# Performance work log

Measured on AMD Instinct MI355X. Metric: run time of the kernel, lower is better.

The kernel has to match this reference:

```python
import jax, jax.numpy as jnp
import numpy as np

EMBED_DIM = 1024
NUM_HEADS = 16
HEAD_DIM = EMBED_DIM // NUM_HEADS


def setup_inputs() -> dict:
    key = jax.random.key(0)
    k1, k2, k3, k4, k5 = jax.random.split(key, 5)
    B, S, D = 2, 2048, EMBED_DIM
    s_in = 1.0 / np.sqrt(D)
    x = jax.random.normal(k1, (B, S, D), dtype=jnp.float32)
    W_qkv = jax.random.uniform(k2, (D, 3 * D), dtype=jnp.float32, minval=-s_in, maxval=s_in)
    b_qkv = jax.random.uniform(k3, (3 * D,), dtype=jnp.float32, minval=-s_in, maxval=s_in)
    W_out = jax.random.uniform(k4, (D, D), dtype=jnp.float32, minval=-s_in, maxval=s_in)
    b_out = jax.random.uniform(k5, (D,), dtype=jnp.float32, minval=-s_in, maxval=s_in)
    return {"x": x, "W_qkv": W_qkv, "b_qkv": b_qkv, "W_out": W_out, "b_out": b_out}


def reference(x, W_qkv, b_qkv, W_out, b_out):
    B, S, D = x.shape
    H, Hd = NUM_HEADS, HEAD_DIM
    qkv = x @ W_qkv + b_qkv                      # [B,S,3D]
    qkv = qkv.reshape(B, S, 3, H, Hd)
    q = qkv[:, :, 0].transpose(0, 2, 1, 3)       # [B,H,S,Hd]
    k = qkv[:, :, 1].transpose(0, 2, 1, 3)
    v = qkv[:, :, 2].transpose(0, 2, 1, 3)
    scores = jnp.einsum('bhsd,bhtd->bhst', q, k) / jnp.sqrt(jnp.float32(Hd))
    attn = jax.nn.softmax(scores, axis=-1)       # dropout is identity in eval mode
    out = jnp.einsum('bhst,bhtd->bhsd', attn, v)
    out = out.transpose(0, 2, 1, 3).reshape(B, S, D)
    return out @ W_out + b_out
```

## Files before the change

### kernel.cpp

```cpp
#include <hip/hip_runtime.h>
#include <stdint.h>
#include <math.h>

#define EMBED 1024
#define HEADS 16
#define HDIM  64
#define SEQ   2048
#define BATCH 2

typedef __bf16 bf16x8 __attribute__((ext_vector_type(8)));
typedef float  f32x4  __attribute__((ext_vector_type(4)));
typedef unsigned short u16x8 __attribute__((ext_vector_type(8)));
typedef unsigned short u16x4 __attribute__((ext_vector_type(4)));
typedef uint32_t u32x4v __attribute__((ext_vector_type(4)));

static __device__ __forceinline__ unsigned short f2bf(float f){
  union { float f; uint32_t u; } v; v.f = f;
  uint32_t u = v.u;
  uint32_t r = (u + 0x7FFFu + ((u >> 16) & 1u)) >> 16;
  return (unsigned short)r;
}
static __device__ __forceinline__ bf16x8 as_bf(u16x8 v){ return __builtin_bit_cast(bf16x8, v); }

static __device__ __forceinline__ uint32_t pk_bf16(float a, float b){
#if defined(__has_builtin) && __has_builtin(__builtin_amdgcn_cvt_pk_bf16_f32)
  typedef __bf16 bf16x2 __attribute__((ext_vector_type(2)));
  bf16x2 p = __builtin_amdgcn_cvt_pk_bf16_f32(a, b);
  return __builtin_bit_cast(uint32_t, p);
#else
  return (uint32_t)f2bf(a) | ((uint32_t)f2bf(b) << 16);
#endif
}

static __device__ __forceinline__ float fexp2(float x){
#if defined(__has_builtin) && __has_builtin(__builtin_amdgcn_exp2f)
  return __builtin_amdgcn_exp2f(x);
#else
  return exp2f(x);
#endif
}

static __device__ __forceinline__ void stage16(const unsigned short* gp,
                                               unsigned short* lp_wave, int lane){
#if defined(__has_builtin) && __has_builtin(__builtin_amdgcn_global_load_lds)
  __builtin_amdgcn_global_load_lds((const __attribute__((address_space(1))) void*)gp,
                                   (__attribute__((address_space(3))) void*)lp_wave,
                                   16, 0, 0);
#else
  *(u16x8*)(lp_wave + lane * 8) = *(const u16x8*)gp;
#endif
}

__global__ __launch_bounds__(256) void cast_x(const float* __restrict__ in,
                                              unsigned short* __restrict__ out){
  int i = (blockIdx.x * 256 + threadIdx.x) * 4;
  float4 v = *(const float4*)(in + i);
  u16x4 o;
  o[0] = f2bf(v.x); o[1] = f2bf(v.y); o[2] = f2bf(v.z); o[3] = f2bf(v.w);
  *(u16x4*)(out + i) = o;
}

__global__ __launch_bounds__(256) void wtrans(const float* __restrict__ W,
                                              unsigned short* __restrict__ Wt,
                                              int N, int K){
  __shared__ unsigned short T[32 * 36];
  int t = threadIdx.x;
  int n0 = blockIdx.x * 32, k0 = blockIdx.y * 32;
  int kr = t >> 3, nc = (t & 7) * 4;
  float4 wv = *(const float4*)(W + (size_t)(k0 + kr) * N + n0 + nc);
  T[(nc + 0) * 36 + kr] = f2bf(wv.x);
  T[(nc + 1) * 36 + kr] = f2bf(wv.y);
  T[(nc + 2) * 36 + kr] = f2bf(wv.z);
  T[(nc + 3) * 36 + kr] = f2bf(wv.w);
  __syncthreads();
  int nr = t >> 3, kc = (t & 7) * 4;
  *(u16x4*)(Wt + (size_t)(n0 + nr) * K + k0 + kc) = *(const u16x4*)&T[nr * 36 + kc];
}

__global__ __launch_bounds__(256) void vtrans(const unsigned short* __restrict__ V,
                                              unsigned short* __restrict__ VT){
  __shared__ unsigned short T[32 * 36];
  int t = threadIdx.x;
  int s0 = blockIdx.x * 32, d0 = blockIdx.y * 32;
  size_t base = (size_t)blockIdx.z * SEQ * HDIM;
  int sr = t >> 3, dc = (t & 7) * 4;
  u16x4 vv = *(const u16x4*)(V + base + (size_t)(s0 + sr) * HDIM + d0 + dc);
  T[(dc + 0) * 36 + sr] = vv[0];
  T[(dc + 1) * 36 + sr] = vv[1];
  T[(dc + 2) * 36 + sr] = vv[2];
  T[(dc + 3) * 36 + sr] = vv[3];
  __syncthreads();
  int dr = t >> 3, sc = (t & 7) * 4;
  int pos = (((sc >> 2) & 3) << 3) + (((sc >> 4) & 1) << 2);
  *(u16x4*)(VT + base + (size_t)(d0 + dr) * SEQ + s0 + pos) = *(const u16x4*)&T[dr * 36 + sc];
}

template<int MODE>
__global__ __launch_bounds__(256) void gemm_bf16(
    const unsigned short* __restrict__ A,
    const unsigned short* __restrict__ Bt,
    const float* __restrict__ bias,
    float* __restrict__ Cout,
    unsigned short* __restrict__ q_ws,
    unsigned short* __restrict__ k_ws,
    unsigned short* __restrict__ v_ws,
    int M, int N, int K)
{
  __shared__ unsigned short As[128 * 32];
  __shared__ unsigned short Bs[128 * 32];
  const int tid  = threadIdx.x;
  const int bm   = blockIdx.y, bn = blockIdx.x;
  const int w    = tid >> 6, lane = tid & 63;
  const int quad = lane >> 4, l16 = lane & 15;
  const int wm   = (w >> 1) * 64, wn = (w & 1) * 64;

  f32x4 acc[4][4] = {};

  for (int k0 = 0; k0 < K; k0 += 32) {
    #pragma unroll
    for (int i = 0; i < 2; i++){
      int c = w + i * 4;
      int row = c * 16 + (lane >> 2);
      int kg = (lane & 3) ^ (row & 3);
      stage16(A  + (size_t)(bm * 128 + row) * K + k0 + kg * 8, &As[c * 512], lane);
      stage16(Bt + (size_t)(bn * 128 + row) * K + k0 + kg * 8, &Bs[c * 512], lane);
    }
    __syncthreads();

    bf16x8 af[4], bfr[4];
    #pragma unroll
    for (int t = 0; t < 4; t++){
      int ra = wm + t * 16 + l16;
      int rb = wn + t * 16 + l16;
      af[t]  = as_bf(*(const u16x8*)&As[(ra << 5) + ((quad ^ (ra & 3)) << 3)]);
      bfr[t] = as_bf(*(const u16x8*)&Bs[(rb << 5) + ((quad ^ (rb & 3)) << 3)]);
    }
    #pragma unroll
    for (int mt = 0; mt < 4; mt++)
      #pragma unroll
      for (int nt = 0; nt < 4; nt++)
        acc[mt][nt] = __builtin_amdgcn_mfma_f32_16x16x32_bf16(af[mt], bfr[nt], acc[mt][nt], 0, 0, 0);
    __syncthreads();
  }

  #pragma unroll
  for (int mt = 0; mt < 4; mt++){
    #pragma unroll
    for (int nt = 0; nt < 4; nt++){
      #pragma unroll
      for (int r = 0; r < 4; r++){
        int gm = bm * 128 + wm + mt * 16 + quad * 4 + r;
        int gn = bn * 128 + wn + nt * 16 + l16;
        float val = acc[mt][nt][r] + bias[gn];
        if (MODE == 0){
          int which = gn >> 10, rem = gn & 1023;
          int h = rem >> 6, hd = rem & 63;
          int b = gm >> 11, s = gm & 2047;
          size_t off = ((size_t)(b * HEADS + h) * SEQ + s) * HDIM + hd;
          if (which == 0)      q_ws[off] = f2bf(val * 0.18033688f);
          else if (which == 1) k_ws[off] = f2bf(val);
          else                 v_ws[off] = f2bf(val);
        } else {
          Cout[(size_t)gm * N + gn] = val;
        }
      }
    }
  }
}

__global__ __launch_bounds__(256) void attn(
    const unsigned short* __restrict__ q_ws,
    const unsigned short* __restrict__ k_ws,
    const unsigned short* __restrict__ vt_ws,
    unsigned short* __restrict__ o_ws)
{
  __shared__ unsigned short Qs[128 * 64];
  __shared__ unsigned short Ks[64 * 64];
  __shared__ unsigned short VTs[64 * 64];
  const int tid  = threadIdx.x;
  const int qt   = blockIdx.x, bh = blockIdx.y;
  const int w    = tid >> 6, lane = tid & 63;
  const int quad = lane >> 4, l16 = lane & 15;
  const size_t base = (size_t)bh * SEQ * HDIM;

  #pragma unroll
  for (int i = 0; i < 4; i++){
    int c = w * 4 + i;
    int row = c * 8 + (lane >> 3);
    int kg = (lane & 7) ^ (row & 7);
    stage16(q_ws + base + (size_t)(qt * 128 + row) * HDIM + kg * 8, &Qs[c * 512], lane);
  }

  int srow[2], skg[2];
  #pragma unroll
  for (int i = 0; i < 2; i++){
    int c = w * 2 + i;
    srow[i] = c * 8 + (lane >> 3);
    skg[i]  = (lane & 7) ^ (srow[i] & 7);
  }

  #pragma unroll
  for (int i = 0; i < 2; i++){
    int c = w * 2 + i;
    stage16(k_ws  + base + (size_t)srow[i] * HDIM + skg[i] * 8, &Ks[c * 512],  lane);
    stage16(vt_ws + base + (size_t)srow[i] * SEQ + skg[i] * 8,  &VTs[c * 512], lane);
  }
  __syncthreads();

  bf16x8 bq[2][2];
  #pragma unroll
  for (int mq = 0; mq < 2; mq++){
    int row = w * 32 + mq * 16 + l16;
    #pragma unroll
    for (int ks = 0; ks < 2; ks++)
      bq[mq][ks] = as_bf(*(const u16x8*)&Qs[(row << 6) + ((((ks << 2) + quad) ^ (row & 7)) << 3)]);
  }

  f32x4 acc[2][4] = {};
  float li[2] = {0.f, 0.f};

  for (int kt = 0; kt < SEQ / 64; kt++){
    u16x8 kpre[2], vpre[2];
    if (kt < SEQ / 64 - 1){
      #pragma unroll
      for (int i = 0; i < 2; i++){
        kpre[i] = *(const u16x8*)(k_ws  + base + (size_t)((kt + 1) * 64 + srow[i]) * HDIM + skg[i] * 8);
        vpre[i] = *(const u16x8*)(vt_ws + base + (size_t)srow[i] * SEQ + (kt + 1) * 64 + skg[i] * 8);
      }
    }

    f32x4 sf[4][2] = {};
    #pragma unroll
    for (int ks = 0; ks < 2; ks++){
      #pragma unroll
      for (int nt = 0; nt < 4; nt++){
        int rk = nt * 16 + l16;
        bf16x8 ak = as_bf(*(const u16x8*)&Ks[(rk << 6) + ((((ks << 2) + quad) ^ (rk & 7)) << 3)]);
        #pragma unroll
        for (int mq = 0; mq < 2; mq++)
          sf[nt][mq] = __builtin_amdgcn_mfma_f32_16x16x32_bf16(ak, bq[mq][ks], sf[nt][mq], 0, 0, 0);
      }
    }

    #pragma unroll
    for (int nt = 0; nt < 4; nt++)
      #pragma unroll
      for (int mq = 0; mq < 2; mq++)
        #pragma unroll
        for (int r = 0; r < 4; r++)
          sf[nt][mq][r] = fexp2(sf[nt][mq][r]);
    #pragma unroll
    for (int mq = 0; mq < 2; mq++)
      #pragma unroll
      for (int nt = 0; nt < 4; nt++)
        li[mq] += (sf[nt][mq][0] + sf[nt][mq][1]) + (sf[nt][mq][2] + sf[nt][mq][3]);

    #pragma unroll
    for (int c = 0; c < 2; c++){
      bf16x8 ap[2];
      #pragma unroll
      for (int mq = 0; mq < 2; mq++){
        u32x4v aw;
        aw[0] = pk_bf16(sf[c * 2][mq][0],     sf[c * 2][mq][1]);
        aw[1] = pk_bf16(sf[c * 2][mq][2],     sf[c * 2][mq][3]);
        aw[2] = pk_bf16(sf[c * 2 + 1][mq][0], sf[c * 2 + 1][mq][1]);
        aw[3] = pk_bf16(sf[c * 2 + 1][mq][2], sf[c * 2 + 1][mq][3]);
        ap[mq] = __builtin_bit_cast(bf16x8, aw);
      }
      #pragma unroll
      for (int nt = 0; nt < 4; nt++){
        int rv = nt * 16 + l16;
        bf16x8 bv = as_bf(*(const u16x8*)&VTs[(rv << 6) + ((((c << 2) + quad) ^ (rv & 7)) << 3)]);
        #pragma unroll
        for (int mq = 0; mq < 2; mq++)
          acc[mq][nt] = __builtin_amdgcn_mfma_f32_16x16x32_bf16(ap[mq], bv, acc[mq][nt], 0, 0, 0);
      }
    }
    __syncthreads();

    if (kt < SEQ / 64 - 1){
      #pragma unroll
      for (int i = 0; i < 2; i++){
        int c = w * 2 + i;
        *(u16x8*)&Ks[c * 512 + lane * 8]  = kpre[i];
        *(u16x8*)&VTs[c * 512 + lane * 8] = vpre[i];
      }
      __syncthreads();
    }
  }

  #pragma unroll
  for (int mq = 0; mq < 2; mq++){
    li[mq] += __shfl_xor(li[mq], 16);
    li[mq] += __shfl_xor(li[mq], 32);
  }
  float inv[2] = {1.0f / li[0], 1.0f / li[1]};
  float invr[2][4];
  #pragma unroll
  for (int mq = 0; mq < 2; mq++)
    #pragma unroll
    for (int r = 0; r < 4; r++)
      invr[mq][r] = __shfl(inv[mq], quad * 4 + r);

  int b = bh >> 4, h = bh & 15;
  #pragma unroll
  for (int mq = 0; mq < 2; mq++)
    #pragma unroll
    for (int nt = 0; nt < 4; nt++)
      #pragma unroll
      for (int r = 0; r < 4; r++){
        int s = qt * 128 + w * 32 + mq * 16 + quad * 4 + r;
        int d = h * 64 + nt * 16 + l16;
        o_ws[((size_t)(b * SEQ + s)) * EMBED + d] = f2bf(acc[mq][nt][r] * invr[mq][r]);
      }
}

extern "C" void kernel_launch(void* const* d_in, const int* in_sizes, int n_in,
                              void* d_out, int out_size, void* d_ws, size_t ws_size,
                              hipStream_t stream) {
  const float* x     = (const float*)d_in[0];
  const float* W_qkv = (const float*)d_in[1];
  const float* b_qkv = (const float*)d_in[2];
  const float* W_out = (const float*)d_in[3];
  const float* b_out = (const float*)d_in[4];
  float* out = (float*)d_out;

  char* ws = (char*)d_ws;
  unsigned short* xb    = (unsigned short*)(ws);
  unsigned short* q     = (unsigned short*)(ws + ((size_t)8  << 20));
  unsigned short* k     = (unsigned short*)(ws + ((size_t)16 << 20));
  unsigned short* v     = (unsigned short*)(ws + ((size_t)24 << 20));
  unsigned short* vt    = (unsigned short*)(ws + ((size_t)32 << 20));
  unsigned short* wqkvT = (unsigned short*)(ws + ((size_t)32 << 20));
  unsigned short* woutT = (unsigned short*)(ws + ((size_t)24 << 20));
  unsigned short* o     = xb;

  cast_x<<<dim3(4096), dim3(256), 0, stream>>>(x, xb);

  wtrans<<<dim3(96, 32), dim3(256), 0, stream>>>(W_qkv, wqkvT, 3072, 1024);

  gemm_bf16<0><<<dim3(24, 32), dim3(256), 0, stream>>>(
      xb, wqkvT, b_qkv, nullptr, q, k, v, 4096, 3072, 1024);

  vtrans<<<dim3(64, 2, 32), dim3(256), 0, stream>>>(v, vt);

  wtrans<<<dim3(32, 32), dim3(256), 0, stream>>>(W_out, woutT, 1024, 1024);

  attn<<<dim3(16, 32), dim3(256), 0, stream>>>(q, k, vt, o);

  gemm_bf16<1><<<dim3(8, 32), dim3(256), 0, stream>>>(
      o, woutT, b_out, out, nullptr, nullptr, nullptr, 4096, 1024, 1024);
}
```

Before: 209.3 us.

## Split attention across 8 waves and narrow output GEMM tiles for occupancy

The attention kernel now runs 512 threads per block, with each wave owning 16 query rows instead of 32. K/V staging is shared across more waves, so each thread issues fewer loads and holds fewer registers. The output projection gets its own kernel with 128x64 tiles, doubling the grid from 256 to 512 blocks so more CUs are busy. The QKV GEMM epilogue hoists the q/k/v destination and scale selection out of the per-element loop. The trade-off is less MFMA work per LDS fragment read and more barrier participants in attention.

```diff
diff --git a/kernel.cpp b/kernel.cpp
--- a/kernel.cpp
+++ b/kernel.cpp
@@ -95,12 +95,10 @@
   *(u16x4*)(VT + base + (size_t)(d0 + dr) * SEQ + s0 + pos) = *(const u16x4*)&T[dr * 36 + sc];
 }
 
-template<int MODE>
-__global__ __launch_bounds__(256) void gemm_bf16(
+__global__ __launch_bounds__(256) void gemm_qkv(
     const unsigned short* __restrict__ A,
     const unsigned short* __restrict__ Bt,
     const float* __restrict__ bias,
-    float* __restrict__ Cout,
     unsigned short* __restrict__ q_ws,
     unsigned short* __restrict__ k_ws,
     unsigned short* __restrict__ v_ws,
@@ -143,6 +141,9 @@
     __syncthreads();
   }
 
+  const int which = (bn * 128) >> 10;
+  unsigned short* dst = (which == 0) ? q_ws : (which == 1) ? k_ws : v_ws;
+  const float scale = (which == 0) ? 0.18033688f : 1.0f;
   #pragma unroll
   for (int mt = 0; mt < 4; mt++){
     #pragma unroll
@@ -151,24 +152,81 @@
       for (int r = 0; r < 4; r++){
         int gm = bm * 128 + wm + mt * 16 + quad * 4 + r;
         int gn = bn * 128 + wn + nt * 16 + l16;
-        float val = acc[mt][nt][r] + bias[gn];
-        if (MODE == 0){
-          int which = gn >> 10, rem = gn & 1023;
-          int h = rem >> 6, hd = rem & 63;
-          int b = gm >> 11, s = gm & 2047;
-          size_t off = ((size_t)(b * HEADS + h) * SEQ + s) * HDIM + hd;
-          if (which == 0)      q_ws[off] = f2bf(val * 0.18033688f);
-          else if (which == 1) k_ws[off] = f2bf(val);
-          else                 v_ws[off] = f2bf(val);
-        } else {
-          Cout[(size_t)gm * N + gn] = val;
-        }
+        int rem = gn & 1023;
+        int h = rem >> 6, hd = rem & 63;
+        int b = gm >> 11, s = gm & 2047;
+        float val = (acc[mt][nt][r] + bias[gn]) * scale;
+        dst[((size_t)(b * HEADS + h) * SEQ + s) * HDIM + hd] = f2bf(val);
       }
     }
   }
 }
 
-__global__ __launch_bounds__(256) void attn(
+__global__ __launch_bounds__(256) void gemm_out(
+    const unsigned short* __restrict__ A,
+    const unsigned short* __restrict__ Bt,
+    const float* __restrict__ bias,
+    float* __restrict__ Cout,
+    int M, int N, int K)
+{
+  __shared__ unsigned short As[128 * 32];
+  __shared__ unsigned short Bs[64 * 32];
+  const int tid  = threadIdx.x;
+  const int bm   = blockIdx.y, bn = blockIdx.x;
+  const int w    = tid >> 6, lane = tid & 63;
+  const int quad = lane >> 4, l16 = lane & 15;
+  const int wm   = (w >> 1) * 64, wn = (w & 1) * 32;
+
+  f32x4 acc[4][2] = {};
+
+  for (int k0 = 0; k0 < K; k0 += 32) {
+    #pragma unroll
+    for (int i = 0; i < 2; i++){
+      int c = w + i * 4;
+      int row = c * 16 + (lane >> 2);
+      int kg = (lane & 3) ^ (row & 3);
+      stage16(A + (size_t)(bm * 128 + row) * K + k0 + kg * 8, &As[c * 512], lane);
+    }
+    {
+      int c = w;
+      int row = c * 16 + (lane >> 2);
+      int kg = (lane & 3) ^ (row & 3);
+      stage16(Bt + (size_t)(bn * 64 + row) * K + k0 + kg * 8, &Bs[c * 512], lane);
+    }
+    __syncthreads();
+
+    bf16x8 af[4], bfr[2];
+    #pragma unroll
+    for (int t = 0; t < 4; t++){
+      int ra = wm + t * 16 + l16;
+      af[t] = as_bf(*(const u16x8*)&As[(ra << 5) + ((quad ^ (ra & 3)) << 3)]);
+    }
+    #pragma unroll
+    for (int t = 0; t < 2; t++){
+      int rb = wn + t * 16 + l16;
+      bfr[t] = as_bf(*(const u16x8*)&Bs[(rb << 5) + ((quad ^ (rb & 3)) << 3)]);
+    }
+    #pragma unroll
+    for (int mt = 0; mt < 4; mt++)
+      #pragma unroll
+      for (int nt = 0; nt < 2; nt++)
+        acc[mt][nt] = __builtin_amdgcn_mfma_f32_16x16x32_bf16(af[mt], bfr[nt], acc[mt][nt], 0, 0, 0);
+    __syncthreads();
+  }
+
+  #pragma unroll
+  for (int mt = 0; mt < 4; mt++)
+    #pragma unroll
+    for (int nt = 0; nt < 2; nt++)
+      #pragma unroll
+      for (int r = 0; r < 4; r++){
+        int gm = bm * 128 + wm + mt * 16 + quad * 4 + r;
+        int gn = bn * 64 + wn + nt * 16 + l16;
+        Cout[(size_t)gm * N + gn] = acc[mt][nt][r] + bias[gn];
+      }
+}
+
+__global__ __launch_bounds__(512) void attn(
     const unsigned short* __restrict__ q_ws,
     const unsigned short* __restrict__ k_ws,
     const unsigned short* __restrict__ vt_ws,
@@ -184,135 +242,99 @@
   const size_t base = (size_t)bh * SEQ * HDIM;
 
   #pragma unroll
-  for (int i = 0; i < 4; i++){
-    int c = w * 4 + i;
+  for (int i = 0; i < 2; i++){
+    int c = w * 2 + i;
     int row = c * 8 + (lane >> 3);
     int kg = (lane & 7) ^ (row & 7);
     stage16(q_ws + base + (size_t)(qt * 128 + row) * HDIM + kg * 8, &Qs[c * 512], lane);
   }
 
-  int srow[2], skg[2];
-  #pragma unroll
-  for (int i = 0; i < 2; i++){
-    int c = w * 2 + i;
-    srow[i] = c * 8 + (lane >> 3);
-    skg[i]  = (lane & 7) ^ (srow[i] & 7);
-  }
-
-  #pragma unroll
-  for (int i = 0; i < 2; i++){
-    int c = w * 2 + i;
-    stage16(k_ws  + base + (size_t)srow[i] * HDIM + skg[i] * 8, &Ks[c * 512],  lane);
-    stage16(vt_ws + base + (size_t)srow[i] * SEQ + skg[i] * 8,  &VTs[c * 512], lane);
-  }
+  const int srow = w * 8 + (lane >> 3);
+  const int skg  = (lane & 7) ^ (srow & 7);
+
+  stage16(k_ws  + base + (size_t)srow * HDIM + skg * 8, &Ks[w * 512],  lane);
+  stage16(vt_ws + base + (size_t)srow * SEQ + skg * 8,  &VTs[w * 512], lane);
   __syncthreads();
 
-  bf16x8 bq[2][2];
-  #pragma unroll
-  for (int mq = 0; mq < 2; mq++){
-    int row = w * 32 + mq * 16 + l16;
+  bf16x8 bq[2];
+  {
+    int row = w * 16 + l16;
     #pragma unroll
     for (int ks = 0; ks < 2; ks++)
-      bq[mq][ks] = as_bf(*(const u16x8*)&Qs[(row << 6) + ((((ks << 2) + quad) ^ (row & 7)) << 3)]);
-  }
-
-  f32x4 acc[2][4] = {};
-  float li[2] = {0.f, 0.f};
+      bq[ks] = as_bf(*(const u16x8*)&Qs[(row << 6) + ((((ks << 2) + quad) ^ (row & 7)) << 3)]);
+  }
+
+  f32x4 acc[4] = {};
+  float li = 0.f;
 
   for (int kt = 0; kt < SEQ / 64; kt++){
-    u16x8 kpre[2], vpre[2];
+    u16x8 kpre, vpre;
     if (kt < SEQ / 64 - 1){
-      #pragma unroll
-      for (int i = 0; i < 2; i++){
-        kpre[i] = *(const u16x8*)(k_ws  + base + (size_t)((kt + 1) * 64 + srow[i]) * HDIM + skg[i] * 8);
-        vpre[i] = *(const u16x8*)(vt_ws + base + (size_t)srow[i] * SEQ + (kt + 1) * 64 + skg[i] * 8);
-      }
-    }
-
-    f32x4 sf[4][2] = {};
+      kpre = *(const u16x8*)(k_ws  + base + (size_t)((kt + 1) * 64 + srow) * HDIM + skg * 8);
+      vpre = *(const u16x8*)(vt_ws + base + (size_t)srow * SEQ + (kt + 1) * 64 + skg * 8);
+    }
+
+    f32x4 sf[4] = {};
     #pragma unroll
     for (int ks = 0; ks < 2; ks++){
       #pragma unroll
       for (int nt = 0; nt < 4; nt++){
         int rk = nt * 16 + l16;
         bf16x8 ak = as_bf(*(const u16x8*)&Ks[(rk << 6) + ((((ks << 2) + quad) ^ (rk & 7)) << 3)]);
-        #pragma unroll
-        for (int mq = 0; mq < 2; mq++)
-          sf[nt][mq] = __builtin_amdgcn_mfma_f32_16x16x32_bf16(ak, bq[mq][ks], sf[nt][mq], 0, 0, 0);
+        sf[nt] = __builtin_amdgcn_mfma_f32_16x16x32_bf16(ak, bq[ks], sf[nt], 0, 0, 0);
       }
     }
 
     #pragma unroll
     for (int nt = 0; nt < 4; nt++)
       #pragma unroll
-      for (int mq = 0; mq < 2; mq++)
-        #pragma unroll
-        for (int r = 0; r < 4; r++)
-          sf[nt][mq][r] = fexp2(sf[nt][mq][r]);
-    #pragma unroll
-    for (int mq = 0; mq < 2; mq++)
-      #pragma unroll
-      for (int nt = 0; nt < 4; nt++)
-        li[mq] += (sf[nt][mq][0] + sf[nt][mq][1]) + (sf[nt][mq][2] + sf[nt][mq][3]);
+      for (int r = 0; r < 4; r++)
+        sf[nt][r] = fexp2(sf[nt][r]);
+    #pragma unroll
+    for (int nt = 0; nt < 4; nt++)
+      li += (sf[nt][0] + sf[nt][1]) + (sf[nt][2] + sf[nt][3]);
 
     #pragma unroll
     for (int c = 0; c < 2; c++){
-      bf16x8 ap[2];
-      #pragma unroll
-      for (int mq = 0; mq < 2; mq++){
-        u32x4v aw;
-        aw[0] = pk_bf16(sf[c * 2][mq][0],     sf[c * 2][mq][1]);
-        aw[1] = pk_bf16(sf[c * 2][mq][2],     sf[c * 2][mq][3]);
-        aw[2] = pk_bf16(sf[c * 2 + 1][mq][0], sf[c * 2 + 1][mq][1]);
-        aw[3] = pk_bf16(sf[c * 2 + 1][mq][2], sf[c * 2 + 1][mq][3]);
-        ap[mq] = __builtin_bit_cast(bf16x8, aw);
-      }
+      u32x4v aw;
+      aw[0] = pk_bf16(sf[c * 2][0],     sf[c * 2][1]);
+      aw[1] = pk_bf16(sf[c * 2][2],     sf[c * 2][3]);
+      aw[2] = pk_bf16(sf[c * 2 + 1][0], sf[c * 2 + 1][1]);
+      aw[3] = pk_bf16(sf[c * 2 + 1][2], sf[c * 2 + 1][3]);
+      bf16x8 ap = __builtin_bit_cast(bf16x8, aw);
       #pragma unroll
       for (int nt = 0; nt < 4; nt++){
         int rv = nt * 16 + l16;
         bf16x8 bv = as_bf(*(const u16x8*)&VTs[(rv << 6) + ((((c << 2) + quad) ^ (rv & 7)) << 3)]);
-        #pragma unroll
-        for (int mq = 0; mq < 2; mq++)
-          acc[mq][nt] = __builtin_amdgcn_mfma_f32_16x16x32_bf16(ap[mq], bv, acc[mq][nt], 0, 0, 0);
+        acc[nt] = __builtin_amdgcn_mfma_f32_16x16x32_bf16(ap, bv, acc[nt], 0, 0, 0);
       }
     }
     __syncthreads();
 
     if (kt < SEQ / 64 - 1){
-      #pragma unroll
-      for (int i = 0; i < 2; i++){
-        int c = w * 2 + i;
-        *(u16x8*)&Ks[c * 512 + lane * 8]  = kpre[i];
-        *(u16x8*)&VTs[c * 512 + lane * 8] = vpre[i];
-      }
+      *(u16x8*)&Ks[w * 512 + lane * 8]  = kpre;
+      *(u16x8*)&VTs[w * 512 + lane * 8] = vpre;
       __syncthreads();
     }
   }
 
-  #pragma unroll
-  for (int mq = 0; mq < 2; mq++){
-    li[mq] += __shfl_xor(li[mq], 16);
-    li[mq] += __shfl_xor(li[mq], 32);
-  }
-  float inv[2] = {1.0f / li[0], 1.0f / li[1]};
-  float invr[2][4];
-  #pragma unroll
-  for (int mq = 0; mq < 2; mq++)
-    #pragma unroll
-    for (int r = 0; r < 4; r++)
-      invr[mq][r] = __shfl(inv[mq], quad * 4 + r);
+  li += __shfl_xor(li, 16);
+  li += __shfl_xor(li, 32);
+  float inv = 1.0f / li;
+  float invr[4];
+  #pragma unroll
+  for (int r = 0; r < 4; r++)
+    invr[r] = __shfl(inv, quad * 4 + r);
 
   int b = bh >> 4, h = bh & 15;
   #pragma unroll
-  for (int mq = 0; mq < 2; mq++)
-    #pragma unroll
-    for (int nt = 0; nt < 4; nt++)
-      #pragma unroll
-      for (int r = 0; r < 4; r++){
-        int s = qt * 128 + w * 32 + mq * 16 + quad * 4 + r;
-        int d = h * 64 + nt * 16 + l16;
-        o_ws[((size_t)(b * SEQ + s)) * EMBED + d] = f2bf(acc[mq][nt][r] * invr[mq][r]);
-      }
+  for (int nt = 0; nt < 4; nt++)
+    #pragma unroll
+    for (int r = 0; r < 4; r++){
+      int s = qt * 128 + w * 16 + quad * 4 + r;
+      int d = h * 64 + nt * 16 + l16;
+      o_ws[((size_t)(b * SEQ + s)) * EMBED + d] = f2bf(acc[nt][r] * invr[r]);
+    }
 }
 
 extern "C" void kernel_launch(void* const* d_in, const int* in_sizes, int n_in,
@@ -339,15 +361,15 @@
 
   wtrans<<<dim3(96, 32), dim3(256), 0, stream>>>(W_qkv, wqkvT, 3072, 1024);
 
-  gemm_bf16<0><<<dim3(24, 32), dim3(256), 0, stream>>>(
-      xb, wqkvT, b_qkv, nullptr, q, k, v, 4096, 3072, 1024);
+  gemm_qkv<<<dim3(24, 32), dim3(256), 0, stream>>>(
+      xb, wqkvT, b_qkv, q, k, v, 4096, 3072, 1024);
 
   vtrans<<<dim3(64, 2, 32), dim3(256), 0, stream>>>(v, vt);
 
   wtrans<<<dim3(32, 32), dim3(256), 0, stream>>>(W_out, woutT, 1024, 1024);
 
-  attn<<<dim3(16, 32), dim3(256), 0, stream>>>(q, k, vt, o);
-
-  gemm_bf16<1><<<dim3(8, 32), dim3(256), 0, stream>>>(
-      o, woutT, b_out, out, nullptr, nullptr, nullptr, 4096, 1024, 1024);
-}
+  attn<<<dim3(16, 32), dim3(512), 0, stream>>>(q, k, vt, o);
+
+  gemm_out<<<dim3(16, 32), dim3(256), 0, stream>>>(
+      o, woutT, b_out, out, 4096, 1024, 1024);
+}
```

Result: faster. 202.4 us (-3.3%).
